# Kernel tuning notes

Measured on AMD Instinct MI355X. Metric: run time of the kernel, lower is better.

Reference implementation:

```python
import jax, jax.numpy as jnp
import numpy as np

EMBED_DIM = 1024
NUM_HEADS = 8
SEQ_LEN = 2048
EPS = 1e-6


def setup_inputs() -> dict:
    key = jax.random.key(0)
    ks = jax.random.split(key, 8)
    E, NH, S = EMBED_DIM, NUM_HEADS, SEQ_LEN
    q = jax.random.normal(ks[0], (S, E), jnp.float32)
    k = jax.random.normal(ks[1], (S, E), jnp.float32)
    v = jax.random.normal(ks[2], (S, E), jnp.float32)
    # gate projections: weights init'd to zeros in the module; use small random
    # values so the gate math is exercised. Biases follow the module's init.
    Wi = 0.02 * jax.random.normal(ks[3], (NH, 3 * E), jnp.float32)
    bi = jnp.linspace(3.0, 6.0, NH, dtype=jnp.float32)
    Wf = 0.02 * jax.random.normal(ks[4], (NH, 3 * E), jnp.float32)
    bf = jnp.sqrt(0.1) * jax.random.normal(ks[5], (NH,), jnp.float32)
    # ResidualLayerNorm (xLSTM-style): effective scale = 1 + weight, no bias
    ln_weight = jnp.zeros((E,), jnp.float32)
    return {"q": q, "k": k, "v": v, "Wi": Wi, "bi": bi, "Wf": Wf, "bf": bf,
            "ln_weight": ln_weight}


def _mlstm_parallel(q, k, v, Wi, bi, Wf, bf, ln_weight):
    S, E = q.shape
    NH = Wi.shape[0]
    DH = E // NH
    gate_in = jnp.concatenate((q, k, v), axis=1)            # (S, 3E)
    ig = (gate_in @ Wi.T + bi).T[:, :, None]                # (NH, S, 1)
    fg = (gate_in @ Wf.T + bf).T[:, :, None]                # (NH, S, 1)

    qh = q.reshape(S, NH, DH).transpose(1, 0, 2)            # (NH, S, DH)
    kh = k.reshape(S, NH, DH).transpose(1, 0, 2)
    vh = v.reshape(S, NH, DH).transpose(1, 0, 2)

    # cumulative log forget gates
    log_f = jax.nn.log_sigmoid(fg)                          # (NH, S, 1)
    log_f_cum = jnp.concatenate(
        [jnp.zeros((NH, 1, 1), q.dtype), jnp.cumsum(log_f, axis=1)], axis=1
    )                                                       # (NH, S+1, 1)
    log_fg_mat = log_f_cum - log_f_cum.transpose(0, 2, 1)   # (NH, S+1, S+1)
    causal = jnp.tril(jnp.ones((S, S), bool))
    log_fg_mat = jnp.where(causal, log_fg_mat[:, 1:, 1:], -jnp.inf)  # (NH,S,S)

    log_D = log_fg_mat + ig.transpose(0, 2, 1)              # (NH, S, S)
    max_log_D = jnp.max(log_D, axis=-1, keepdims=True)      # (NH, S, 1)
    D = jnp.exp(log_D - max_log_D)                          # stabilized

    qk = jnp.einsum('hsd,htd->hst', qh, kh) / jnp.sqrt(jnp.asarray(DH, q.dtype))
    C = qk * D                                              # (NH, S, S)
    normalizer = jnp.maximum(jnp.abs(jnp.sum(C, axis=-1, keepdims=True)),
                             jnp.exp(-max_log_D))
    C_norm = C / (normalizer + EPS)
    h = jnp.einsum('hst,htd->hsd', C_norm, vh)              # (NH, S, DH)
    h = h.transpose(1, 0, 2).reshape(S, E)

    # residual layer norm: LN(h) * (1 + weight), no bias
    mu = jnp.mean(h, axis=-1, keepdims=True)
    var = jnp.mean(jnp.square(h - mu), axis=-1, keepdims=True)
    h_norm = (h - mu) * jax.lax.rsqrt(var + 1e-5)
    return h_norm * (1.0 + ln_weight)


def reference(q, k, v, Wi, bi, Wf, bf, ln_weight):
    return _mlstm_parallel(q, k, v, Wi, bi, Wf, bf, ln_weight)
```

## Files before the change

kernel.cpp:

```cpp
#include <hip/hip_runtime.h>
#include <math.h>

#define S_LEN 2048
#define EMB   1024
#define NHEAD 8
#define DH    128
#define E3    3072
#define BM    64
#define BN    32
#define NSPLIT 4
#define TPB   4
#define NGB   (S_LEN / TPB)
#define PTSTRIDE 40

typedef __bf16 bf16x8 __attribute__((ext_vector_type(8)));
typedef __bf16 bf16x4 __attribute__((ext_vector_type(4)));
typedef float  f32x4  __attribute__((ext_vector_type(4)));

__device__ __forceinline__ void gload16(const __bf16* g, __bf16* l) {
    __builtin_amdgcn_global_load_lds(
        (const __attribute__((address_space(1))) void*)g,
        (__attribute__((address_space(3))) void*)l, 16, 0, 0);
}

__global__ __launch_bounds__(256) void gates_cvt_transpose_kernel(
    const float* __restrict__ q, const float* __restrict__ k,
    const float* __restrict__ v,
    const float* __restrict__ Wi, const float* __restrict__ bi,
    const float* __restrict__ Wf, const float* __restrict__ bf,
    __bf16* __restrict__ Qh, __bf16* __restrict__ Ql,
    __bf16* __restrict__ Kh, __bf16* __restrict__ Kl,
    __bf16* __restrict__ Vt,
    float* __restrict__ ig, float* __restrict__ lf)
{
    const int tid = threadIdx.x;
    __shared__ union {
        float red[16][TPB][4];
        __bf16 tile[32][33];
    } sh;

    if (blockIdx.x < NGB) {
        const int t0 = blockIdx.x * TPB;
        float4 qv[TPB], kv[TPB], vv[TPB];
        #pragma unroll
        for (int t = 0; t < TPB; ++t) {
            qv[t] = ((const float4*)q)[(size_t)(t0 + t) * 256 + tid];
            kv[t] = ((const float4*)k)[(size_t)(t0 + t) * 256 + tid];
            vv[t] = ((const float4*)v)[(size_t)(t0 + t) * 256 + tid];
        }
        #pragma unroll
        for (int t = 0; t < TPB; ++t) {
            size_t idx = (size_t)(t0 + t) * 256 + tid;
            bf16x4 hi, lo;
            hi[0]=(__bf16)qv[t].x; hi[1]=(__bf16)qv[t].y; hi[2]=(__bf16)qv[t].z; hi[3]=(__bf16)qv[t].w;
            lo[0]=(__bf16)(qv[t].x-(float)hi[0]); lo[1]=(__bf16)(qv[t].y-(float)hi[1]);
            lo[2]=(__bf16)(qv[t].z-(float)hi[2]); lo[3]=(__bf16)(qv[t].w-(float)hi[3]);
            ((bf16x4*)Qh)[idx] = hi; ((bf16x4*)Ql)[idx] = lo;
            hi[0]=(__bf16)kv[t].x; hi[1]=(__bf16)kv[t].y; hi[2]=(__bf16)kv[t].z; hi[3]=(__bf16)kv[t].w;
            lo[0]=(__bf16)(kv[t].x-(float)hi[0]); lo[1]=(__bf16)(kv[t].y-(float)hi[1]);
            lo[2]=(__bf16)(kv[t].z-(float)hi[2]); lo[3]=(__bf16)(kv[t].w-(float)hi[3]);
            ((bf16x4*)Kh)[idx] = hi; ((bf16x4*)Kl)[idx] = lo;
        }
        float acc[16][TPB];
        #pragma unroll
        for (int g = 0; g < 16; ++g) {
            const float4* w4 = (const float4*)((g < 8) ? (Wi + g * E3) : (Wf + (g - 8) * E3));
            float4 a = w4[tid], b = w4[256 + tid], c = w4[512 + tid];
            #pragma unroll
            for (int t = 0; t < TPB; ++t) {
                acc[g][t] = a.x*qv[t].x + a.y*qv[t].y + a.z*qv[t].z + a.w*qv[t].w
                          + b.x*kv[t].x + b.y*kv[t].y + b.z*kv[t].z + b.w*kv[t].w
                          + c.x*vv[t].x + c.y*vv[t].y + c.z*vv[t].z + c.w*vv[t].w;
            }
        }
        const int w = tid >> 6, lane = tid & 63;
        #pragma unroll
        for (int g = 0; g < 16; ++g) {
            #pragma unroll
            for (int t = 0; t < TPB; ++t) {
                float x = acc[g][t];
                for (int o = 32; o > 0; o >>= 1) x += __shfl_down(x, o, 64);
                if (lane == 0) sh.red[g][t][w] = x;
            }
        }
        __syncthreads();
        if (tid < 16 * TPB) {
            const int g = tid >> 2, t = tid & (TPB - 1);
            float s = sh.red[g][t][0] + sh.red[g][t][1] + sh.red[g][t][2] + sh.red[g][t][3];
            if (g < 8) {
                ig[g * S_LEN + t0 + t] = s + bi[g];
            } else {
                int h = g - 8;
                float x = s + bf[h];
                lf[h * S_LEN + t0 + t] = fminf(x, 0.f) - log1pf(expf(-fabsf(x)));
            }
        }
    } else {
        const int tb = blockIdx.x - NGB;
        const int sb = (tb & 63) * 32, eb = (tb >> 6) * 32;
        #pragma unroll
        for (int i = 0; i < 4; ++i) {
            int lin = tid + i * 256;
            int sr = lin >> 5, ec = lin & 31;
            sh.tile[ec][sr] = (__bf16)v[(size_t)(sb + sr) * EMB + eb + ec];
        }
        __syncthreads();
        #pragma unroll
        for (int i = 0; i < 4; ++i) {
            int lin = tid + i * 256;
            int er = lin >> 5, sc = lin & 31;
            Vt[(size_t)(eb + er) * S_LEN + sb + sc] = sh.tile[er][sc];
        }
    }
}

__global__ __launch_bounds__(256) void cumsum_aux_kernel(
    const float* __restrict__ lf, const float* __restrict__ ig,
    float* __restrict__ F, float* __restrict__ ug,
    float* __restrict__ umax, float* __restrict__ upmax)
{
    const int h = blockIdx.x, tid = threadIdx.x;
    const int lane = tid & 63, w = tid >> 6;
    __shared__ float wsum[4];
    __shared__ float morig[256];
    float loc[8];
    const int base = tid * 8;
    float s = 0.f;
    for (int i = 0; i < 8; i++) { s += lf[h * S_LEN + base + i]; loc[i] = s; }
    float inc = s;
    #pragma unroll
    for (int o = 1; o < 64; o <<= 1) {
        float t = __shfl_up(inc, o, 64);
        if (lane >= o) inc += t;
    }
    if (lane == 63) wsum[w] = inc;
    __syncthreads();
    float wpre = 0.f;
    #pragma unroll
    for (int i = 0; i < 4; ++i) if (i < w) wpre += wsum[i];
    const float prev = wpre + inc - s;
    float* Fh = F + h * (S_LEN + 1);
    if (tid == 0) Fh[0] = 0.f;
    float Fv[8];
    for (int i = 0; i < 8; i++) { Fv[i] = prev + loc[i]; Fh[base + i + 1] = Fv[i]; }

    const float* igh = ig + h * S_LEN;
    float pm[8];
    float runm = -1e30f;
    #pragma unroll
    for (int i = 0; i < 8; i++) {
        float u = igh[base + i] - Fv[i];
        ug[h * S_LEN + base + i] = u;
        runm = fmaxf(runm, u);
        pm[i] = runm;
    }
    morig[tid] = runm;
    __syncthreads();
    const int g0 = tid & ~3;
    float pfx = -1e30f;
    for (int j = g0; j < tid; ++j) pfx = fmaxf(pfx, morig[j]);
    #pragma unroll
    for (int i = 0; i < 8; i++)
        upmax[h * S_LEN + base + i] = fmaxf(pfx, pm[i]);
    if ((tid & 3) == 0) {
        float mm = fmaxf(fmaxf(morig[tid], morig[tid + 1]),
                         fmaxf(morig[tid + 2], morig[tid + 3]));
        umax[h * 64 + (tid >> 2)] = mm;
    }
}

__global__ __launch_bounds__(256, 2) void mlstm_mfma(
    const __bf16* __restrict__ Qhg, const __bf16* __restrict__ Qlg,
    const __bf16* __restrict__ Khg, const __bf16* __restrict__ Klg,
    const __bf16* __restrict__ Vtg,
    const float* __restrict__ ug, const float* __restrict__ umaxg,
    const float* __restrict__ upmaxg, const float* __restrict__ F,
    __bf16* __restrict__ Opart, float* __restrict__ msplit,
    float* __restrict__ lsplit)
{
    const int flat = blockIdx.x;
    const int h = flat & 7;
    const int rest = flat >> 3;
    const int xx = rest & 15, z = rest >> 4;
    const int tid  = threadIdx.x;
    const int lane = tid & 63, w = tid >> 6;
    const int quad = lane >> 4, l15 = lane & 15;

    __shared__ __bf16 KhL[2][4096];
    __shared__ __bf16 KlL[2][4096];
    __shared__ __bf16 VtL[2][4096];
    __shared__ __bf16 Pt[4][16 * PTSTRIDE];

    const float* Fh  = F  + h * (S_LEN + 1);
    const float* ugh = ug + h * S_LEN;
    const float scale = 0.088388347648318447f;

    const int krow0 = tid >> 4;
    const int krow1 = 16 + krow0;
    const int kchk  = (tid & 15) ^ (krow0 & 15);
    const int vrow0 = tid >> 2;
    const int vrow1 = 64 + vrow0;
    const int vchk  = (tid & 3) ^ ((vrow0 ^ (vrow0 >> 2)) & 3);
    const int ldsw  = w * 512;

#define STAGE(B, TB) do {                                                     \
    const __bf16* kb_ = Khg + (size_t)(TB) * EMB + h * DH;                    \
    const __bf16* lb_ = Klg + (size_t)(TB) * EMB + h * DH;                    \
    const __bf16* vg_ = Vtg + (size_t)(h * DH) * S_LEN + (TB);                \
    gload16(kb_ + (size_t)krow0 * EMB + kchk * 8, &KhL[B][ldsw]);             \
    gload16(kb_ + (size_t)krow1 * EMB + kchk * 8, &KhL[B][2048 + ldsw]);      \
    gload16(lb_ + (size_t)krow0 * EMB + kchk * 8, &KlL[B][ldsw]);             \
    gload16(lb_ + (size_t)krow1 * EMB + kchk * 8, &KlL[B][2048 + ldsw]);      \
    gload16(vg_ + (size_t)vrow0 * S_LEN + vchk * 8, &VtL[B][ldsw]);           \
    gload16(vg_ + (size_t)vrow1 * S_LEN + vchk * 8, &VtL[B][2048 + ldsw]);    \
} while (0)

    for (int pair = 0; pair < 2; ++pair) {
        const int qt = (pair == 0) ? xx : 31 - xx;
        const int qb = qt * BM;
        const int nj = 2 * qt + 2;
        const int j0 = (z * nj) / NSPLIT, j1 = ((z + 1) * nj) / NSPLIT;
        const int qbw = qb + w * 16;
        const int SBLK = (qb >> 5) + (w >> 1);

        float fq[4], upm[4];
        int sglob[4];
        #pragma unroll
        for (int r = 0; r < 4; ++r) {
            int s = qbw + quad * 4 + r;
            sglob[r] = s;
            fq[r]  = Fh[s + 1];
            upm[r] = upmaxg[h * S_LEN + s];
        }

        bf16x8 qh[4], ql[4];
        {
            const size_t qrow = (size_t)(qbw + l15) * EMB + h * DH + quad * 8;
            #pragma unroll
            for (int kk = 0; kk < 4; ++kk) {
                qh[kk] = *(const bf16x8*)(Qhg + qrow + kk * 32);
                ql[kk] = *(const bf16x8*)(Qlg + qrow + kk * 32);
            }
        }
        #pragma unroll
        for (int kk = 0; kk < 4; ++kk)
            asm volatile("" : "+v"(qh[kk]), "+v"(ql[kk]));

        float m_r[4] = {-1e30f, -1e30f, -1e30f, -1e30f};
        float l_r[4] = {0.f, 0.f, 0.f, 0.f};
        f32x4 Oacc[8] = {{0,0,0,0},{0,0,0,0},{0,0,0,0},{0,0,0,0},
                         {0,0,0,0},{0,0,0,0},{0,0,0,0},{0,0,0,0}};

        float pu0 = 0.f, pu1 = 0.f, pum = 0.f;
        int buf = 0;
        if (j0 < j1) {
            STAGE(0, j0 * BN);
            pu0 = ugh[j0 * BN + l15];
            pu1 = ugh[j0 * BN + 16 + l15];
            pum = umaxg[h * 64 + j0];
            __syncthreads();
        }

        for (int j = j0; j < j1; ++j) {
            const int tb = j * BN;
            const float ut0 = pu0, ut1 = pu1, umj = pum;
            if (j + 1 < j1) {
                STAGE(buf ^ 1, tb + BN);
                pu0 = ugh[tb + BN + l15];
                pu1 = ugh[tb + BN + 16 + l15];
                pum = umaxg[h * 64 + (j + 1)];
            }
            if (j <= SBLK) {
                f32x4 S0 = {0,0,0,0}, S1 = {0,0,0,0};
                #pragma unroll
                for (int kk = 0; kk < 4; ++kk) {
                    const int kpos = (((kk << 2) | quad) ^ l15) * 8;
                    bf16x8 bh0 = *(const bf16x8*)&KhL[buf][l15 * 128 + kpos];
                    bf16x8 bl0 = *(const bf16x8*)&KlL[buf][l15 * 128 + kpos];
                    S0 = __builtin_amdgcn_mfma_f32_16x16x32_bf16(qh[kk], bh0, S0, 0, 0, 0);
                    S0 = __builtin_amdgcn_mfma_f32_16x16x32_bf16(qh[kk], bl0, S0, 0, 0, 0);
                    S0 = __builtin_amdgcn_mfma_f32_16x16x32_bf16(ql[kk], bh0, S0, 0, 0, 0);
                    bf16x8 bh1 = *(const bf16x8*)&KhL[buf][(16 + l15) * 128 + kpos];
                    bf16x8 bl1 = *(const bf16x8*)&KlL[buf][(16 + l15) * 128 + kpos];
                    S1 = __builtin_amdgcn_mfma_f32_16x16x32_bf16(qh[kk], bh1, S1, 0, 0, 0);
                    S1 = __builtin_amdgcn_mfma_f32_16x16x32_bf16(qh[kk], bl1, S1, 0, 0, 0);
                    S1 = __builtin_amdgcn_mfma_f32_16x16x32_bf16(ql[kk], bh1, S1, 0, 0, 0);
                }
                const int t0 = tb + l15, t1 = tb + 16 + l15;
                #pragma unroll
                for (int r = 0; r < 4; ++r) {
                    float mt = (j < SBLK) ? (fq[r] + umj) : (fq[r] + upm[r]);
                    float mn = fmaxf(m_r[r], mt);
                    float alpha = __expf(m_r[r] - mn);
                    m_r[r] = mn;
                    #pragma unroll
                    for (int nt = 0; nt < 8; ++nt) Oacc[nt][r] *= alpha;
                    float p0 = __expf(fq[r] + ut0 - mn) * S0[r] * scale;
                    float p1 = __expf(fq[r] + ut1 - mn) * S1[r] * scale;
                    if (j == SBLK) {
                        if (t0 > sglob[r]) p0 = 0.f;
                        if (t1 > sglob[r]) p1 = 0.f;
                    }
                    l_r[r] = l_r[r] * alpha + (p0 + p1);
                    const int prow = (quad * 4 + r) * PTSTRIDE;
                    Pt[w][prow + l15]      = (__bf16)p0;
                    Pt[w][prow + 16 + l15] = (__bf16)p1;
                }
                bf16x8 pa = *(const bf16x8*)&Pt[w][l15 * PTSTRIDE + quad * 8];
                #pragma unroll
                for (int nt = 0; nt < 8; ++nt) {
                    const int vrow = nt * 16 + l15;
                    const int vpos = (quad ^ ((vrow ^ (vrow >> 2)) & 3)) * 8;
                    bf16x8 vv = *(const bf16x8*)&VtL[buf][vrow * 32 + vpos];
                    Oacc[nt] = __builtin_amdgcn_mfma_f32_16x16x32_bf16(pa, vv, Oacc[nt], 0, 0, 0);
                }
            }
            __syncthreads();
            buf ^= 1;
        }
        __bf16* Oz = Opart + (size_t)z * S_LEN * EMB;
        #pragma unroll
        for (int nt = 0; nt < 8; ++nt) {
            #pragma unroll
            for (int r = 0; r < 4; ++r) {
                Oz[(size_t)sglob[r] * EMB + h * DH + nt * 16 + l15] = (__bf16)Oacc[nt][r];
            }
        }
        #pragma unroll
        for (int r = 0; r < 4; ++r) {
            float x = l_r[r];
            #pragma unroll
            for (int o = 1; o < 16; o <<= 1) x += __shfl_xor(x, o);
            l_r[r] = x;
        }
        if (l15 == 0) {
            #pragma unroll
            for (int r = 0; r < 4; ++r) {
                msplit[(z * NHEAD + h) * S_LEN + sglob[r]] = m_r[r];
                lsplit[(z * NHEAD + h) * S_LEN + sglob[r]] = l_r[r];
            }
        }
    }
#undef STAGE
}

__global__ __launch_bounds__(256) void combine_ln_kernel(
    const __bf16* __restrict__ Opart, const float* __restrict__ msplit,
    const float* __restrict__ lsplit, const float* __restrict__ lnw,
    float* __restrict__ out)
{
    const int tid = threadIdx.x;
    const int r  = tid >> 7;
    const int wr = (tid >> 6) & 1;
    const int c0 = (tid & 127) * 8;
    const int hh = c0 >> 7;
    const int s  = blockIdx.x * 2 + r;
    __shared__ float redsum[2][2], redvar[2][2];

    float m = -1e30f, es[NSPLIT], l = 0.f;
    #pragma unroll
    for (int zz = 0; zz < NSPLIT; ++zz)
        m = fmaxf(m, msplit[(zz * NHEAD + hh) * S_LEN + s]);
    #pragma unroll
    for (int zz = 0; zz < NSPLIT; ++zz) {
        es[zz] = __expf(msplit[(zz * NHEAD + hh) * S_LEN + s] - m);
        l += es[zz] * lsplit[(zz * NHEAD + hh) * S_LEN + s];
    }
    const float rn = 1.f / (fmaxf(fabsf(l), __expf(-m)) + 1e-6f);

    const size_t SE = (size_t)S_LEN * EMB;
    float x[8] = {0,0,0,0,0,0,0,0};
    #pragma unroll
    for (int zz = 0; zz < NSPLIT; ++zz) {
        if (es[zz] != 0.f) {
            bf16x8 o = *(const bf16x8*)(Opart + zz * SE + (size_t)s * EMB + c0);
            #pragma unroll
            for (int e = 0; e < 8; ++e) x[e] += es[zz] * (float)o[e];
        }
    }
    float sum = 0.f;
    #pragma unroll
    for (int e = 0; e < 8; ++e) { x[e] *= rn; sum += x[e]; }
    for (int o = 32; o > 0; o >>= 1) sum += __shfl_down(sum, o, 64);
    if ((tid & 63) == 0) redsum[r][wr] = sum;
    __syncthreads();
    sum = redsum[r][0] + redsum[r][1];
    const float mu = sum * (1.f / EMB);
    float vs = 0.f;
    #pragma unroll
    for (int e = 0; e < 8; ++e) { float d = x[e] - mu; vs += d * d; }
    for (int o = 32; o > 0; o >>= 1) vs += __shfl_down(vs, o, 64);
    if ((tid & 63) == 0) redvar[r][wr] = vs;
    __syncthreads();
    vs = redvar[r][0] + redvar[r][1];
    const float rstd = rsqrtf(vs * (1.f / EMB) + 1e-5f);
    const float4 w0 = *(const float4*)(lnw + c0);
    const float4 w1 = *(const float4*)(lnw + c0 + 4);
    float4 o0, o1;
    o0.x = (x[0]-mu)*rstd*(1.f+w0.x); o0.y = (x[1]-mu)*rstd*(1.f+w0.y);
    o0.z = (x[2]-mu)*rstd*(1.f+w0.z); o0.w = (x[3]-mu)*rstd*(1.f+w0.w);
    o1.x = (x[4]-mu)*rstd*(1.f+w1.x); o1.y = (x[5]-mu)*rstd*(1.f+w1.y);
    o1.z = (x[6]-mu)*rstd*(1.f+w1.z); o1.w = (x[7]-mu)*rstd*(1.f+w1.w);
    *(float4*)(out + (size_t)s * EMB + c0)     = o0;
    *(float4*)(out + (size_t)s * EMB + c0 + 4) = o1;
}

extern "C" void kernel_launch(void* const* d_in, const int* in_sizes, int n_in,
                              void* d_out, int out_size, void* d_ws, size_t ws_size,
                              hipStream_t stream)
{
    const float* q   = (const float*)d_in[0];
    const float* k   = (const float*)d_in[1];
    const float* v   = (const float*)d_in[2];
    const float* Wi  = (const float*)d_in[3];
    const float* bi  = (const float*)d_in[4];
    const float* Wf  = (const float*)d_in[5];
    const float* bf  = (const float*)d_in[6];
    const float* lnw = (const float*)d_in[7];
    float* out = (float*)d_out;

    float* ws = (float*)d_ws;
    float* ig    = ws;
    float* lf    = ig + NHEAD * S_LEN;
    float* F     = lf + NHEAD * S_LEN;
    float* ugw   = F + NHEAD * (S_LEN + 1);
    float* umaxw = ugw + NHEAD * S_LEN;
    float* upmaxw= umaxw + NHEAD * 64;
    __bf16* Qh = (__bf16*)(upmaxw + NHEAD * S_LEN);
    const size_t SEb = (size_t)S_LEN * EMB;
    __bf16* Ql  = Qh + SEb;
    __bf16* Kh  = Ql + SEb;
    __bf16* Kl  = Kh + SEb;
    __bf16* Vtg = Kl + SEb;
    __bf16* Opart = Vtg + SEb;
    float* msplit = (float*)(Opart + (size_t)NSPLIT * SEb);
    float* lsplit = msplit + NSPLIT * NHEAD * S_LEN;

    gates_cvt_transpose_kernel<<<NGB + 2048, 256, 0, stream>>>(
        q, k, v, Wi, bi, Wf, bf, Qh, Ql, Kh, Kl, Vtg, ig, lf);
    cumsum_aux_kernel<<<NHEAD, 256, 0, stream>>>(lf, ig, F, ugw, umaxw, upmaxw);
    mlstm_mfma<<<16 * NHEAD * NSPLIT, 256, 0, stream>>>(
        Qh, Ql, Kh, Kl, Vtg, ugw, umaxw, upmaxw, F, Opart, msplit, lsplit);
    combine_ln_kernel<<<S_LEN / 2, 256, 0, stream>>>(Opart, msplit, lsplit, lnw, out);
}
```

Measured before the change: 149.9 us.

## Split V transpose into its own kernel and single-buffer V tile in LDS

Moves the V transpose blocks out of the gates kernel into a separate launch, and changes the attention loop so the V tile is single-buffered. V is now loaded at the start of each iteration, with an extra barrier between building P and the PV MFMA. This lowers LDS use per block, which may allow more resident blocks, at the cost of an added synchronisation and less prefetch overlap for V. It also adds one kernel launch.

```diff
diff --git a/kernel.cpp b/kernel.cpp
--- a/kernel.cpp
+++ b/kernel.cpp
@@ -23,94 +23,94 @@
         (__attribute__((address_space(3))) void*)l, 16, 0, 0);
 }
 
-__global__ __launch_bounds__(256) void gates_cvt_transpose_kernel(
+__global__ __launch_bounds__(256) void gates_kernel(
     const float* __restrict__ q, const float* __restrict__ k,
     const float* __restrict__ v,
     const float* __restrict__ Wi, const float* __restrict__ bi,
     const float* __restrict__ Wf, const float* __restrict__ bf,
     __bf16* __restrict__ Qh, __bf16* __restrict__ Ql,
     __bf16* __restrict__ Kh, __bf16* __restrict__ Kl,
-    __bf16* __restrict__ Vt,
     float* __restrict__ ig, float* __restrict__ lf)
 {
     const int tid = threadIdx.x;
-    __shared__ union {
-        float red[16][TPB][4];
-        __bf16 tile[32][33];
-    } sh;
-
-    if (blockIdx.x < NGB) {
-        const int t0 = blockIdx.x * TPB;
-        float4 qv[TPB], kv[TPB], vv[TPB];
+    __shared__ float red[16][TPB][4];
+
+    const int t0 = blockIdx.x * TPB;
+    float4 qv[TPB], kv[TPB], vv[TPB];
+    #pragma unroll
+    for (int t = 0; t < TPB; ++t) {
+        qv[t] = ((const float4*)q)[(size_t)(t0 + t) * 256 + tid];
+        kv[t] = ((const float4*)k)[(size_t)(t0 + t) * 256 + tid];
+        vv[t] = ((const float4*)v)[(size_t)(t0 + t) * 256 + tid];
+    }
+    #pragma unroll
+    for (int t = 0; t < TPB; ++t) {
+        size_t idx = (size_t)(t0 + t) * 256 + tid;
+        bf16x4 hi, lo;
+        hi[0]=(__bf16)qv[t].x; hi[1]=(__bf16)qv[t].y; hi[2]=(__bf16)qv[t].z; hi[3]=(__bf16)qv[t].w;
+        lo[0]=(__bf16)(qv[t].x-(float)hi[0]); lo[1]=(__bf16)(qv[t].y-(float)hi[1]);
+        lo[2]=(__bf16)(qv[t].z-(float)hi[2]); lo[3]=(__bf16)(qv[t].w-(float)hi[3]);
+        ((bf16x4*)Qh)[idx] = hi; ((bf16x4*)Ql)[idx] = lo;
+        hi[0]=(__bf16)kv[t].x; hi[1]=(__bf16)kv[t].y; hi[2]=(__bf16)kv[t].z; hi[3]=(__bf16)kv[t].w;
+        lo[0]=(__bf16)(kv[t].x-(float)hi[0]); lo[1]=(__bf16)(kv[t].y-(float)hi[1]);
+        lo[2]=(__bf16)(kv[t].z-(float)hi[2]); lo[3]=(__bf16)(kv[t].w-(float)hi[3]);
+        ((bf16x4*)Kh)[idx] = hi; ((bf16x4*)Kl)[idx] = lo;
+    }
+    float acc[16][TPB];
+    #pragma unroll
+    for (int g = 0; g < 16; ++g) {
+        const float4* w4 = (const float4*)((g < 8) ? (Wi + g * E3) : (Wf + (g - 8) * E3));
+        float4 a = w4[tid], b = w4[256 + tid], c = w4[512 + tid];
         #pragma unroll
         for (int t = 0; t < TPB; ++t) {
-            qv[t] = ((const float4*)q)[(size_t)(t0 + t) * 256 + tid];
-            kv[t] = ((const float4*)k)[(size_t)(t0 + t) * 256 + tid];
-            vv[t] = ((const float4*)v)[(size_t)(t0 + t) * 256 + tid];
-        }
+            acc[g][t] = a.x*qv[t].x + a.y*qv[t].y + a.z*qv[t].z + a.w*qv[t].w
+                      + b.x*kv[t].x + b.y*kv[t].y + b.z*kv[t].z + b.w*kv[t].w
+                      + c.x*vv[t].x + c.y*vv[t].y + c.z*vv[t].z + c.w*vv[t].w;
+        }
+    }
+    const int w = tid >> 6, lane = tid & 63;
+    #pragma unroll
+    for (int g = 0; g < 16; ++g) {
         #pragma unroll
         for (int t = 0; t < TPB; ++t) {
-            size_t idx = (size_t)(t0 + t) * 256 + tid;
-            bf16x4 hi, lo;
-            hi[0]=(__bf16)qv[t].x; hi[1]=(__bf16)qv[t].y; hi[2]=(__bf16)qv[t].z; hi[3]=(__bf16)qv[t].w;
-            lo[0]=(__bf16)(qv[t].x-(float)hi[0]); lo[1]=(__bf16)(qv[t].y-(float)hi[1]);
-            lo[2]=(__bf16)(qv[t].z-(float)hi[2]); lo[3]=(__bf16)(qv[t].w-(float)hi[3]);
-            ((bf16x4*)Qh)[idx] = hi; ((bf16x4*)Ql)[idx] = lo;
-            hi[0]=(__bf16)kv[t].x; hi[1]=(__bf16)kv[t].y; hi[2]=(__bf16)kv[t].z; hi[3]=(__bf16)kv[t].w;
-            lo[0]=(__bf16)(kv[t].x-(float)hi[0]); lo[1]=(__bf16)(kv[t].y-(float)hi[1]);
-            lo[2]=(__bf16)(kv[t].z-(float)hi[2]); lo[3]=(__bf16)(kv[t].w-(float)hi[3]);
-            ((bf16x4*)Kh)[idx] = hi; ((bf16x4*)Kl)[idx] = lo;
-        }
-        float acc[16][TPB];
-        #pragma unroll
-        for (int g = 0; g < 16; ++g) {
-            const float4* w4 = (const float4*)((g < 8) ? (Wi + g * E3) : (Wf + (g - 8) * E3));
-            float4 a = w4[tid], b = w4[256 + tid], c = w4[512 + tid];
-            #pragma unroll
-            for (int t = 0; t < TPB; ++t) {
-                acc[g][t] = a.x*qv[t].x + a.y*qv[t].y + a.z*qv[t].z + a.w*qv[t].w
-                          + b.x*kv[t].x + b.y*kv[t].y + b.z*kv[t].z + b.w*kv[t].w
-                          + c.x*vv[t].x + c.y*vv[t].y + c.z*vv[t].z + c.w*vv[t].w;
-            }
-        }
-        const int w = tid >> 6, lane = tid & 63;
-        #pragma unroll
-        for (int g = 0; g < 16; ++g) {
-            #pragma unroll
-            for (int t = 0; t < TPB; ++t) {
-                float x = acc[g][t];
-                for (int o = 32; o > 0; o >>= 1) x += __shfl_down(x, o, 64);
-                if (lane == 0) sh.red[g][t][w] = x;
-            }
-        }
-        __syncthreads();
-        if (tid < 16 * TPB) {
-            const int g = tid >> 2, t = tid & (TPB - 1);
-            float s = sh.red[g][t][0] + sh.red[g][t][1] + sh.red[g][t][2] + sh.red[g][t][3];
-            if (g < 8) {
-                ig[g * S_LEN + t0 + t] = s + bi[g];
-            } else {
-                int h = g - 8;
-                float x = s + bf[h];
-                lf[h * S_LEN + t0 + t] = fminf(x, 0.f) - log1pf(expf(-fabsf(x)));
-            }
-        }
-    } else {
-        const int tb = blockIdx.x - NGB;
-        const int sb = (tb & 63) * 32, eb = (tb >> 6) * 32;
-        #pragma unroll
-        for (int i = 0; i < 4; ++i) {
-            int lin = tid + i * 256;
-            int sr = lin >> 5, ec = lin & 31;
-            sh.tile[ec][sr] = (__bf16)v[(size_t)(sb + sr) * EMB + eb + ec];
-        }
-        __syncthreads();
-        #pragma unroll
-        for (int i = 0; i < 4; ++i) {
-            int lin = tid + i * 256;
-            int er = lin >> 5, sc = lin & 31;
-            Vt[(size_t)(eb + er) * S_LEN + sb + sc] = sh.tile[er][sc];
-        }
+            float x = acc[g][t];
+            for (int o = 32; o > 0; o >>= 1) x += __shfl_down(x, o, 64);
+            if (lane == 0) red[g][t][w] = x;
+        }
+    }
+    __syncthreads();
+    if (tid < 16 * TPB) {
+        const int g = tid >> 2, t = tid & (TPB - 1);
+        float s = red[g][t][0] + red[g][t][1] + red[g][t][2] + red[g][t][3];
+        if (g < 8) {
+            ig[g * S_LEN + t0 + t] = s + bi[g];
+        } else {
+            int h = g - 8;
+            float x = s + bf[h];
+            lf[h * S_LEN + t0 + t] = fminf(x, 0.f) - log1pf(expf(-fabsf(x)));
+        }
+    }
+}
+
+__global__ __launch_bounds__(256) void vtrans_kernel(
+    const float* __restrict__ v, __bf16* __restrict__ Vt)
+{
+    const int tid = threadIdx.x;
+    __shared__ __bf16 tile[32][33];
+    const int tb = blockIdx.x;
+    const int sb = (tb & 63) * 32, eb = (tb >> 6) * 32;
+    #pragma unroll
+    for (int i = 0; i < 4; ++i) {
+        int lin = tid + i * 256;
+        int sr = lin >> 5, ec = lin & 31;
+        tile[ec][sr] = (__bf16)v[(size_t)(sb + sr) * EMB + eb + ec];
+    }
+    __syncthreads();
+    #pragma unroll
+    for (int i = 0; i < 4; ++i) {
+        int lin = tid + i * 256;
+        int er = lin >> 5, sc = lin & 31;
+        Vt[(size_t)(eb + er) * S_LEN + sb + sc] = tile[er][sc];
     }
 }
 
@@ -188,7 +188,7 @@
 
     __shared__ __bf16 KhL[2][4096];
     __shared__ __bf16 KlL[2][4096];
-    __shared__ __bf16 VtL[2][4096];
+    __shared__ __bf16 VtL[4096];
     __shared__ __bf16 Pt[4][16 * PTSTRIDE];
 
     const float* Fh  = F  + h * (S_LEN + 1);
@@ -203,16 +203,18 @@
     const int vchk  = (tid & 3) ^ ((vrow0 ^ (vrow0 >> 2)) & 3);
     const int ldsw  = w * 512;
 
-#define STAGE(B, TB) do {                                                     \
+#define STAGE_K(B, TB) do {                                                   \
     const __bf16* kb_ = Khg + (size_t)(TB) * EMB + h * DH;                    \
     const __bf16* lb_ = Klg + (size_t)(TB) * EMB + h * DH;                    \
-    const __bf16* vg_ = Vtg + (size_t)(h * DH) * S_LEN + (TB);                \
     gload16(kb_ + (size_t)krow0 * EMB + kchk * 8, &KhL[B][ldsw]);             \
     gload16(kb_ + (size_t)krow1 * EMB + kchk * 8, &KhL[B][2048 + ldsw]);      \
     gload16(lb_ + (size_t)krow0 * EMB + kchk * 8, &KlL[B][ldsw]);             \
     gload16(lb_ + (size_t)krow1 * EMB + kchk * 8, &KlL[B][2048 + ldsw]);      \
-    gload16(vg_ + (size_t)vrow0 * S_LEN + vchk * 8, &VtL[B][ldsw]);           \
-    gload16(vg_ + (size_t)vrow1 * S_LEN + vchk * 8, &VtL[B][2048 + ldsw]);    \
+} while (0)
+#define STAGE_V(TB) do {                                                      \
+    const __bf16* vg_ = Vtg + (size_t)(h * DH) * S_LEN + (TB);                \
+    gload16(vg_ + (size_t)vrow0 * S_LEN + vchk * 8, &VtL[ldsw]);              \
+    gload16(vg_ + (size_t)vrow1 * S_LEN + vchk * 8, &VtL[2048 + ldsw]);       \
 } while (0)
 
     for (int pair = 0; pair < 2; ++pair) {
@@ -254,7 +256,7 @@
         float pu0 = 0.f, pu1 = 0.f, pum = 0.f;
         int buf = 0;
         if (j0 < j1) {
-            STAGE(0, j0 * BN);
+            STAGE_K(0, j0 * BN);
             pu0 = ugh[j0 * BN + l15];
             pu1 = ugh[j0 * BN + 16 + l15];
             pum = umaxg[h * 64 + j0];
@@ -263,9 +265,10 @@
 
         for (int j = j0; j < j1; ++j) {
             const int tb = j * BN;
+            STAGE_V(tb);
+            if (j + 1 < j1) STAGE_K(buf ^ 1, tb + BN);
             const float ut0 = pu0, ut1 = pu1, umj = pum;
             if (j + 1 < j1) {
-                STAGE(buf ^ 1, tb + BN);
                 pu0 = ugh[tb + BN + l15];
                 pu1 = ugh[tb + BN + 16 + l15];
                 pum = umaxg[h * 64 + (j + 1)];
@@ -306,12 +309,15 @@
                     Pt[w][prow + l15]      = (__bf16)p0;
                     Pt[w][prow + 16 + l15] = (__bf16)p1;
                 }
+            }
+            __syncthreads();
+            if (j <= SBLK) {
                 bf16x8 pa = *(const bf16x8*)&Pt[w][l15 * PTSTRIDE + quad * 8];
                 #pragma unroll
                 for (int nt = 0; nt < 8; ++nt) {
                     const int vrow = nt * 16 + l15;
                     const int vpos = (quad ^ ((vrow ^ (vrow >> 2)) & 3)) * 8;
-                    bf16x8 vv = *(const bf16x8*)&VtL[buf][vrow * 32 + vpos];
+                    bf16x8 vv = *(const bf16x8*)&VtL[vrow * 32 + vpos];
                     Oacc[nt] = __builtin_amdgcn_mfma_f32_16x16x32_bf16(pa, vv, Oacc[nt], 0, 0, 0);
                 }
             }
@@ -341,7 +347,8 @@
             }
         }
     }
-#undef STAGE
+#undef STAGE_K
+#undef STAGE_V
 }
 
 __global__ __launch_bounds__(256) void combine_ln_kernel(
@@ -436,8 +443,9 @@
     float* msplit = (float*)(Opart + (size_t)NSPLIT * SEb);
     float* lsplit = msplit + NSPLIT * NHEAD * S_LEN;
 
-    gates_cvt_transpose_kernel<<<NGB + 2048, 256, 0, stream>>>(
-        q, k, v, Wi, bi, Wf, bf, Qh, Ql, Kh, Kl, Vtg, ig, lf);
+    gates_kernel<<<NGB, 256, 0, stream>>>(
+        q, k, v, Wi, bi, Wf, bf, Qh, Ql, Kh, Kl, ig, lf);
+    vtrans_kernel<<<2048, 256, 0, stream>>>(v, Vtg);
     cumsum_aux_kernel<<<NHEAD, 256, 0, stream>>>(lf, ig, F, ugw, umaxw, upmaxw);
     mlstm_mfma<<<16 * NHEAD * NSPLIT, 256, 0, stream>>>(
         Qh, Ql, Kh, Kl, Vtg, ugw, umaxw, upmaxw, F, Opart, msplit, lsplit);
```

New measurement: 148.5 us. Within noise of the previous version (-0.9%).
